# Kernel optimization log

Hardware: AMD Instinct MI355X
Metric: run time of the kernel (lower is better)

Reference implementation:

```python
import jax, jax.numpy as jnp
import numpy as np

# dims
N = 50000          # nodes
E = 400000         # edges
R = 32             # radial basis
F = 132            # features_dim
EV = 15            # sum(2l+1) for degrees [1,2,3]
H_INV, D_INV = 4, 33
H_EV, D_EV = 3, 44
REPEATS = np.array([3, 5, 7])            # 2l+1 per degree
ATT_NORM_INV = float(np.sqrt(D_INV))
ATT_NORM_EV = float(np.sqrt(D_EV))

# degree contraction matrix: (x*x) @ M sums squared m-components per degree -> [.., 3]
M_L0 = np.zeros((EV, 3), np.float32)
_off = 0
for _i, _r in enumerate(REPEATS):
    M_L0[_off:_off + _r, _i] = 1.0
    _off += _r
M_L0 = jnp.asarray(M_L0)


def _filter_net(rbf, ev_inv, rW1, rb1, rW2, rb2, eW1, eb1, eW2, eb2):
    # FilterNet with num_layers=2: silu(Linear) -> Linear(identity), same for ev path
    a = jax.nn.silu(rbf @ rW1 + rb1) @ rW2 + rb2
    e = jax.nn.silu(ev_inv @ eW1 + eb1) @ eW2 + eb2
    return a + e


def setup_inputs() -> dict:
    key = jax.random.key(0)
    ks = jax.random.split(key, 40)
    p = lambda i, shp, s=0.1: jax.random.normal(ks[i], shp, jnp.float32) * s
    inp = {
        'inv_features': jax.random.normal(ks[0], (N, F), jnp.float32),
        'ev_features': jax.random.normal(ks[1], (N, EV), jnp.float32),
        'rbf': jax.random.uniform(ks[2], (E, R), jnp.float32),
        'sh_vectors': jax.random.normal(ks[3], (E, EV), jnp.float32),
        'cutoffs': jax.random.uniform(ks[4], (E, 1), jnp.float32),
        'senders': jax.random.randint(ks[5], (E,), 0, N),
        'receivers': jax.random.randint(ks[6], (E,), 0, N),
        # attention weights
        'Wq_inv': p(7, (H_INV, D_INV, D_INV)),
        'Wk_inv': p(8, (H_INV, D_INV, D_INV)),
        'Wv_inv': p(9, (H_INV, D_INV, D_INV)),
        'Wq_ev': p(10, (H_EV, D_EV, D_EV)),
        'Wk_ev': p(11, (H_EV, D_EV, D_EV)),
        # filter net (inv branch)
        'fi_rW1': p(12, (R, F)), 'fi_rb1': p(13, (F,)),
        'fi_rW2': p(14, (F, F)), 'fi_rb2': p(15, (F,)),
        'fi_eW1': p(16, (3, F // 4)), 'fi_eb1': p(17, (F // 4,)),
        'fi_eW2': p(18, (F // 4, F)), 'fi_eb2': p(19, (F,)),
        # filter net (ev branch)
        'fe_rW1': p(20, (R, F)), 'fe_rb1': p(21, (F,)),
        'fe_rW2': p(22, (F, F)), 'fe_rb2': p(23, (F,)),
        'fe_eW1': p(24, (3, F // 4)), 'fe_eb1': p(25, (F // 4,)),
        'fe_eW2': p(26, (F // 4, F)), 'fe_eb2': p(27, (F,)),
        # interaction block linear: (F + len(degrees)) -> (F + len(degrees))
        'W_int': p(28, (F + 3, F + 3)), 'b_int': p(29, (F + 3,)),
    }
    return inp


def reference(inv_features, ev_features, rbf, sh_vectors, cutoffs,
              Wq_inv, Wk_inv, Wv_inv, Wq_ev, Wk_ev,
              fi_rW1, fi_rb1, fi_rW2, fi_rb2, fi_eW1, fi_eb1, fi_eW2, fi_eb2,
              fe_rW1, fe_rb1, fe_rW2, fe_rb2, fe_eW1, fe_eb1, fe_eW2, fe_eb2,
              W_int, b_int, senders, receivers):
    n = inv_features.shape[0]

    # --- Euclidean attention block ---
    ev_diff = ev_features[senders] - ev_features[receivers]          # [E, 15]
    ev_diff_inv = (ev_diff * ev_diff) @ M_L0                          # [E, 3] L0 contraction

    fw_inv = _filter_net(rbf, ev_diff_inv, fi_rW1, fi_rb1, fi_rW2, fi_rb2,
                         fi_eW1, fi_eb1, fi_eW2, fi_eb2).reshape(-1, H_INV, D_INV)
    fw_ev = _filter_net(rbf, ev_diff_inv, fe_rW1, fe_rb1, fe_rW2, fe_rb2,
                        fe_eW1, fe_eb1, fe_eW2, fe_eb2).reshape(-1, H_EV, D_EV)

    x_inv = inv_features.reshape(n, H_INV, D_INV)
    x_ev = inv_features.reshape(n, H_EV, D_EV)

    q_inv = jax.nn.silu(jnp.einsum('nhd,hde->nhe', x_inv, Wq_inv))[receivers]
    k_inv = jax.nn.silu(jnp.einsum('nhd,hde->nhe', x_inv, Wk_inv))[senders]
    v_inv = jnp.einsum('nhd,hde->nhe', x_inv, Wv_inv)[senders]
    q_ev = jax.nn.silu(jnp.einsum('nhd,hde->nhe', x_ev, Wq_ev))[receivers]
    k_ev = jax.nn.silu(jnp.einsum('nhd,hde->nhe', x_ev, Wk_ev))[senders]

    alpha_inv = (q_inv * k_inv * fw_inv).sum(-1) / ATT_NORM_INV       # [E, 4]
    alpha_ev = (q_ev * k_ev * fw_ev).sum(-1) / ATT_NORM_EV            # [E, 3]

    msg_inv = cutoffs[:, :, None] * alpha_inv[..., None] * v_inv      # [E, 4, 33]
    d_inv = jax.ops.segment_sum(msg_inv, receivers, num_segments=n).reshape(n, F)

    alpha_ev_full = jnp.repeat(alpha_ev, REPEATS, axis=-1, total_repeat_length=EV)
    msg_ev = cutoffs * alpha_ev_full * sh_vectors                      # [E, 15]
    d_ev = jax.ops.segment_sum(msg_ev, receivers, num_segments=n)

    inv1 = inv_features + d_inv
    ev1 = ev_features + d_ev

    # --- Interaction block ---
    ev1_inv = (ev1 * ev1) @ M_L0                                       # [N, 3]
    t = jnp.concatenate([inv1, ev1_inv], axis=-1) @ W_int + b_int      # [N, 135]
    d_inv2, b_ev = t[:, :F], t[:, F:]
    d_ev2 = jnp.repeat(b_ev, REPEATS, axis=-1, total_repeat_length=EV) * ev1

    return (inv1 + d_inv2, ev1 + d_ev2)
```

## Files before the change

### kernel.cpp

```cpp
#include <hip/hip_runtime.h>
#include <type_traits>

#define N_NODES 50000
#define N_EDGES 400000
#define R_DIM   32
#define F_DIM   132
#define EV_DIM  15
#define F_Q     33
#define INT_DIM 135
#define TE      32
#define NPB     32

#define RCP_NORM_INV 0.17407765595569785f
#define RCP_NORM_EV  0.15075567228888181f

typedef __attribute__((ext_vector_type(8))) short bf16x8;
typedef __attribute__((ext_vector_type(4))) float f32x4;

__device__ __forceinline__ float silu_f(float x) { return x / (1.f + __expf(-x)); }

__device__ __forceinline__ unsigned short f2bf(float x) {
    union { float f; unsigned u; } c; c.f = x;
    unsigned r = c.u + 0x7FFFu + ((c.u >> 16) & 1u);
    return (unsigned short)(r >> 16);
}

__device__ __forceinline__ float bf2f(unsigned short x) {
    union { unsigned u; float f; } c; c.u = (unsigned)x << 16;
    return c.f;
}

__global__ __launch_bounds__(256) void prep_w2_kernel(
    const float* __restrict__ fi_rW2, const float* __restrict__ fi_eW2,
    const float* __restrict__ fe_rW2, const float* __restrict__ fe_eW2,
    const float* __restrict__ fi_rb2, const float* __restrict__ fi_eb2,
    const float* __restrict__ fe_rb2, const float* __restrict__ fe_eb2,
    unsigned short* __restrict__ Bfrag, float* __restrict__ biasC)
{
    int t = blockIdx.x * 256 + threadIdx.x;
    if (t < 6912) {
        int l = t & 63, idx = t >> 6;
        int nt = idx % 9, kc = (idx / 9) % 6, f = idx / 54;
        const float* rW2 = f ? fe_rW2 : fi_rW2;
        const float* eW2 = f ? fe_eW2 : fi_eW2;
        int n = nt * 16 + (l & 15);
        unsigned short v[8];
        #pragma unroll
        for (int j = 0; j < 8; ++j) {
            int k = kc * 32 + (l >> 4) * 8 + j;
            float w = 0.f;
            if (n < F_DIM) {
                if (k < F_DIM) w = rW2[k * F_DIM + n];
                else if (k < F_DIM + F_Q) w = eW2[(k - F_DIM) * F_DIM + n];
            }
            v[j] = f2bf(w);
        }
        *(uint4*)&Bfrag[(size_t)t * 8] = *(const uint4*)v;
    }
    if (blockIdx.x == 0) {
        for (int i = threadIdx.x; i < 288; i += 256) {
            int f = i / 144, n = i % 144;
            const float* rb2 = f ? fe_rb2 : fi_rb2;
            const float* eb2 = f ? fe_eb2 : fi_eb2;
            biasC[i] = (n < F_DIM) ? (rb2[n] + eb2[n]) : 0.f;
        }
    }
}

__global__ __launch_bounds__(256) void prep_aux_kernel(
    const float* __restrict__ fi_rW1, const float* __restrict__ fe_rW1,
    const float* __restrict__ fi_rb1, const float* __restrict__ fi_eb1,
    const float* __restrict__ fe_rb1, const float* __restrict__ fe_eb1,
    const float* __restrict__ Wq_inv, const float* __restrict__ Wk_inv,
    const float* __restrict__ Wv_inv,
    const float* __restrict__ Wq_ev, const float* __restrict__ Wk_ev,
    unsigned short* __restrict__ B1frag, float* __restrict__ biasB1,
    unsigned short* __restrict__ Bnp)
{
    int t = blockIdx.x * 256 + threadIdx.x;
    if (t < 1536) {
        int l = t & 63, idx = t >> 6;
        int nt = idx % 12, f = idx / 12;
        const float* rW1 = f ? fe_rW1 : fi_rW1;
        int n = nt * 16 + (l & 15);
        unsigned short v[8];
        #pragma unroll
        for (int j = 0; j < 8; ++j) {
            int k = (l >> 4) * 8 + j;
            float w = (n < F_DIM) ? rW1[k * F_DIM + n] : 0.f;
            v[j] = f2bf(w);
        }
        *(uint4*)&B1frag[(size_t)t * 8] = *(const uint4*)v;
    } else if (t < 1920) {
        int i = t - 1536;
        int f = i / 192, n = i % 192;
        const float* rb1 = f ? fe_rb1 : fi_rb1;
        const float* eb1 = f ? fe_eb1 : fi_eb1;
        biasB1[i] = (n < F_DIM) ? rb1[n] : ((n < 165) ? eb1[n - F_DIM] : 0.f);
    } else if (t < 1920 + 6912) {
        int u = t - 1920;
        int l = u & 63, blk = u >> 6;
        int n = 0; const float* W = nullptr; int D = 0, h = 0, kc = 0;
        if (blk < 72) {
            int arr = blk / 24, wb = blk % 24;
            h = wb / 6; kc = (wb % 6) / 3; int nt = wb % 3;
            W = (arr == 0) ? Wq_inv : (arr == 1) ? Wk_inv : Wv_inv;
            D = 33; n = nt * 16 + (l & 15);
            W += h * 1089;
        } else {
            int b2 = blk - 72;
            int which = b2 / 18, wb = b2 % 18;
            h = wb / 6; kc = (wb % 6) / 3; int nt = wb % 3;
            W = which ? Wk_ev : Wq_ev;
            D = 44; n = nt * 16 + (l & 15);
            W += h * 1936;
        }
        unsigned short v[8];
        #pragma unroll
        for (int j = 0; j < 8; ++j) {
            int k = kc * 32 + (l >> 4) * 8 + j;
            float w = (k < D && n < D) ? W[k * D + n] : 0.f;
            v[j] = f2bf(w);
        }
        *(uint4*)&Bnp[(size_t)u * 8] = *(const uint4*)v;
    }
}

__global__ __launch_bounds__(256) void hist_kernel(
    const int* __restrict__ receivers, int* __restrict__ cnt)
{
    int i = blockIdx.x * 256 + threadIdx.x;
    if (i < N_EDGES) atomicAdd(&cnt[receivers[i]], 1);
}

__global__ __launch_bounds__(1024) void scan_tile_sum(
    const int* __restrict__ cnt, int* __restrict__ tsum)
{
    int idx = blockIdx.x * 1024 + threadIdx.x;
    int v = (idx < N_NODES) ? cnt[idx] : 0;
    for (int o = 32; o > 0; o >>= 1) v += __shfl_down(v, o);
    __shared__ int wsum[16];
    if ((threadIdx.x & 63) == 0) wsum[threadIdx.x >> 6] = v;
    __syncthreads();
    if (threadIdx.x == 0) {
        int s = 0;
        for (int i = 0; i < 16; ++i) s += wsum[i];
        tsum[blockIdx.x] = s;
    }
}

__global__ __launch_bounds__(64) void scan_base(
    const int* __restrict__ tsum, int* __restrict__ tbase)
{
    if (threadIdx.x == 0) {
        int run = 0;
        for (int i = 0; i < 49; ++i) { tbase[i] = run; run += tsum[i]; }
    }
}

__global__ __launch_bounds__(1024) void scan_tile(
    const int* __restrict__ cnt, const int* __restrict__ tbase,
    int* __restrict__ off, int* __restrict__ cursor)
{
    __shared__ int s[1024];
    int t = threadIdx.x;
    int idx = blockIdx.x * 1024 + t;
    int v = (idx < N_NODES) ? cnt[idx] : 0;
    s[t] = v;
    __syncthreads();
    for (int d = 1; d < 1024; d <<= 1) {
        int x = (t >= d) ? s[t - d] : 0;
        __syncthreads();
        s[t] += x;
        __syncthreads();
    }
    int o = tbase[blockIdx.x] + s[t] - v;
    if (idx < N_NODES) { off[idx] = o; cursor[idx] = o; }
    if (idx == 0) off[N_NODES] = N_EDGES;
}

__global__ __launch_bounds__(256) void scatter_kernel(
    const int* __restrict__ receivers, int* __restrict__ cursor,
    int* __restrict__ perm)
{
    int i = blockIdx.x * 256 + threadIdx.x;
    if (i < N_EDGES) {
        int pos = atomicAdd(&cursor[receivers[i]], 1);
        perm[pos] = i;
    }
}

__global__ __launch_bounds__(256) void node_proj_kernel(
    const float* __restrict__ x,
    const unsigned short* __restrict__ Bnp,
    unsigned short* __restrict__ q_inv, unsigned short* __restrict__ k_inv,
    float* __restrict__ v_inv,
    unsigned short* __restrict__ q_ev, unsigned short* __restrict__ k_ev)
{
    __shared__ __align__(16) unsigned short sx[NPB][456];
    const int node0 = blockIdx.x * NPB;
    const int tid = threadIdx.x;
    for (int i = tid; i < NPB * 448; i += 256) {
        int nd = i / 448, t = i % 448;
        int seg = t >> 6, d = t & 63;
        float v = 0.f;
        int gn = node0 + nd;
        if (gn < N_NODES) {
            if (seg < 4) { if (d < 33) v = x[(size_t)gn * F_DIM + seg * 33 + d]; }
            else         { int h = seg - 4; if (d < 44) v = x[(size_t)gn * F_DIM + h * 44 + d]; }
        }
        sx[nd][t] = f2bf(v);
    }
    __syncthreads();
    const int wv = tid >> 6, l = tid & 63, l15 = l & 15, g4 = l >> 4;
    const int half = wv & 1, m0 = (wv >> 1) * 16;
    const unsigned short* arow = &sx[m0 + l15][0];
    const unsigned short* Bl = Bnp + (size_t)l * 8;

    auto do_qk = [&](int arr, unsigned short* __restrict__ out) {
        const unsigned short* Ba = Bl + (size_t)arr * 24 * 512;
        #pragma unroll
        for (int h = 0; h < 4; ++h) {
            bf16x8 a0 = *(const bf16x8*)&arow[h * 64 + g4 * 8];
            bf16x8 a1 = *(const bf16x8*)&arow[h * 64 + 32 + g4 * 8];
            #pragma unroll
            for (int nt = 0; nt < 3; ++nt) {
                f32x4 c = {0.f, 0.f, 0.f, 0.f};
                c = __builtin_amdgcn_mfma_f32_16x16x32_bf16(
                        a0, *(const bf16x8*)(Ba + (size_t)((h * 2 + 0) * 3 + nt) * 512), c, 0, 0, 0);
                c = __builtin_amdgcn_mfma_f32_16x16x32_bf16(
                        a1, *(const bf16x8*)(Ba + (size_t)((h * 2 + 1) * 3 + nt) * 512), c, 0, 0, 0);
                int e = nt * 16 + l15;
                if (e < 33) {
                    #pragma unroll
                    for (int r = 0; r < 4; ++r) {
                        int gn = node0 + m0 + g4 * 4 + r;
                        if (gn < N_NODES)
                            out[(size_t)gn * F_DIM + h * 33 + e] = f2bf(silu_f(c[r]));
                    }
                }
            }
        }
    };
    auto do_v = [&](float* __restrict__ out) {
        const unsigned short* Ba = Bl + (size_t)2 * 24 * 512;
        #pragma unroll
        for (int h = 0; h < 4; ++h) {
            bf16x8 a0 = *(const bf16x8*)&arow[h * 64 + g4 * 8];
            bf16x8 a1 = *(const bf16x8*)&arow[h * 64 + 32 + g4 * 8];
            #pragma unroll
            for (int nt = 0; nt < 3; ++nt) {
                f32x4 c = {0.f, 0.f, 0.f, 0.f};
                c = __builtin_amdgcn_mfma_f32_16x16x32_bf16(
                        a0, *(const bf16x8*)(Ba + (size_t)((h * 2 + 0) * 3 + nt) * 512), c, 0, 0, 0);
                c = __builtin_amdgcn_mfma_f32_16x16x32_bf16(
                        a1, *(const bf16x8*)(Ba + (size_t)((h * 2 + 1) * 3 + nt) * 512), c, 0, 0, 0);
                int e = nt * 16 + l15;
                if (e < 33) {
                    #pragma unroll
                    for (int r = 0; r < 4; ++r) {
                        int gn = node0 + m0 + g4 * 4 + r;
                        if (gn < N_NODES)
                            out[(size_t)gn * F_DIM + h * 33 + e] = c[r];
                    }
                }
            }
        }
    };
    auto do_ev = [&](int which, unsigned short* __restrict__ out) {
        const unsigned short* Ba = Bl + (size_t)(72 + which * 18) * 512;
        #pragma unroll
        for (int h = 0; h < 3; ++h) {
            bf16x8 a0 = *(const bf16x8*)&arow[256 + h * 64 + g4 * 8];
            bf16x8 a1 = *(const bf16x8*)&arow[256 + h * 64 + 32 + g4 * 8];
            #pragma unroll
            for (int nt = 0; nt < 3; ++nt) {
                f32x4 c = {0.f, 0.f, 0.f, 0.f};
                c = __builtin_amdgcn_mfma_f32_16x16x32_bf16(
                        a0, *(const bf16x8*)(Ba + (size_t)((h * 2 + 0) * 3 + nt) * 512), c, 0, 0, 0);
                c = __builtin_amdgcn_mfma_f32_16x16x32_bf16(
                        a1, *(const bf16x8*)(Ba + (size_t)((h * 2 + 1) * 3 + nt) * 512), c, 0, 0, 0);
                int e = nt * 16 + l15;
                if (e < 44) {
                    #pragma unroll
                    for (int r = 0; r < 4; ++r) {
                        int gn = node0 + m0 + g4 * 4 + r;
                        if (gn < N_NODES)
                            out[(size_t)gn * F_DIM + h * 44 + e] = f2bf(silu_f(c[r]));
                    }
                }
            }
        }
    };
    if (half == 0) { do_qk(0, q_inv); do_qk(1, k_inv); }
    else           { do_v(v_inv); do_ev(0, q_ev); do_ev(1, k_ev); }
}

__global__ __launch_bounds__(256) void edge_alpha_kernel(
    const float* __restrict__ ev_feat, const float* __restrict__ rbf,
    const float* __restrict__ cutoffs,
    const int* __restrict__ senders, const int* __restrict__ receivers,
    const int* __restrict__ perm,
    const float* __restrict__ fi_eW1, const float* __restrict__ fe_eW1,
    const unsigned short* __restrict__ B1frag, const float* __restrict__ biasB1,
    const unsigned short* __restrict__ Bfrag, const float* __restrict__ biasC,
    const unsigned short* __restrict__ q_inv, const unsigned short* __restrict__ k_inv,
    const unsigned short* __restrict__ q_ev, const unsigned short* __restrict__ k_ev,
    float* __restrict__ galpha, int* __restrict__ gsnd)
{
    __shared__ __align__(16) unsigned short s_hid[2][TE][200];
    __shared__ __align__(16) unsigned short s_ain[TE][40];
    __shared__ float s_d2[TE][16];
    __shared__ float s_ei[3][TE];
    __shared__ float s_c[TE];
    __shared__ int s_snd[TE], s_rcv[TE], s_eid[TE];

    const int e0g = blockIdx.x * TE;
    const int tid = threadIdx.x;

    if (tid < TE) {
        int eid = perm[e0g + tid];
        s_eid[tid] = eid;
        int sn = senders[eid], rc = receivers[eid];
        s_snd[tid] = sn; s_rcv[tid] = rc;
        s_c[tid] = cutoffs[eid];
        gsnd[e0g + tid] = sn;
    }
    __syncthreads();
    for (int i = tid; i < TE * R_DIM; i += 256) {
        int e = i >> 5, k = i & 31;
        s_ain[e][k] = f2bf(rbf[(size_t)s_eid[e] * R_DIM + k]);
    }
    for (int i = tid; i < TE * EV_DIM; i += 256) {
        int e = i / EV_DIM, j = i - e * EV_DIM;
        float d = ev_feat[(size_t)s_snd[e] * EV_DIM + j]
                - ev_feat[(size_t)s_rcv[e] * EV_DIM + j];
        s_d2[e][j] = d * d;
    }
    __syncthreads();
    if (tid < TE * 3) {
        int e = tid / 3, k2 = tid - e * 3;
        int i0 = (k2 == 0) ? 0 : (k2 == 1) ? 3 : 8;
        int i1 = (k2 == 0) ? 3 : (k2 == 1) ? 8 : 15;
        float s = 0.f;
        for (int i = i0; i < i1; ++i) s += s_d2[e][i];
        s_ei[k2][e] = s;
    }
    __syncthreads();

    const int wv = tid >> 6, l = tid & 63;
    const int f = wv & 1, m0 = (wv >> 1) * 16;
    const int l15 = l & 15, g4 = l >> 4;

    int rcvr[4], sndr[4];
    #pragma unroll
    for (int r = 0; r < 4; ++r) {
        int e = m0 + g4 * 4 + r;
        rcvr[r] = s_rcv[e]; sndr[r] = s_snd[e];
    }

    {
        bf16x8 a1 = *(const bf16x8*)&s_ain[m0 + l15][g4 * 8];
        const unsigned short* B1f = B1frag + (size_t)f * 6144 + (size_t)l * 8;
        const float* eW1f = f ? fe_eW1 : fi_eW1;
        #pragma unroll
        for (int nt = 0; nt < 12; ++nt) {
            f32x4 c = {0.f, 0.f, 0.f, 0.f};
            bf16x8 b1 = *(const bf16x8*)(B1f + (size_t)nt * 512);
            c = __builtin_amdgcn_mfma_f32_16x16x32_bf16(a1, b1, c, 0, 0, 0);
            const int n = nt * 16 + l15;
            const float bias = biasB1[f * 192 + n];
            float w0 = 0.f, w1 = 0.f, w2 = 0.f;
            if (n >= F_DIM && n < 165) {
                w0 = eW1f[n - F_DIM];
                w1 = eW1f[F_Q + n - F_DIM];
                w2 = eW1f[2 * F_Q + n - F_DIM];
            }
            #pragma unroll
            for (int r = 0; r < 4; ++r) {
                int e = m0 + g4 * 4 + r;
                float eic = w0 * s_ei[0][e] + w1 * s_ei[1][e] + w2 * s_ei[2][e];
                float v = silu_f(c[r] + bias + eic);
                s_hid[f][e][n] = f2bf(v);
            }
        }
    }

    bf16x8 afr[6];
    {
        const unsigned short* hrow = &s_hid[f][m0 + l15][0];
        #pragma unroll
        for (int kc = 0; kc < 6; ++kc)
            afr[kc] = *(const bf16x8*)&hrow[kc * 32 + g4 * 8];
    }
    const unsigned short* Bf = Bfrag + (size_t)f * 54 * 512 + (size_t)l * 8;

    auto run = [&](auto FC) {
        constexpr int F_ = decltype(FC)::value;
        constexpr int NH = F_ ? 3 : 4;
        constexpr int DD = F_ ? 44 : 33;
        const unsigned short* qp = F_ ? q_ev : q_inv;
        const unsigned short* kp = F_ ? k_ev : k_inv;
        float part[NH][4];
        #pragma unroll
        for (int h = 0; h < NH; ++h)
            #pragma unroll
            for (int r = 0; r < 4; ++r) part[h][r] = 0.f;

        auto ldtile = [&](int nt, float (&bq)[4], float (&bk)[4]) {
            const int n = nt * 16 + l15;
            #pragma unroll
            for (int r = 0; r < 4; ++r) {
                float qv = 0.f, kv = 0.f;
                if (n < F_DIM) {
                    qv = bf2f(qp[(size_t)rcvr[r] * F_DIM + n]);
                    kv = bf2f(kp[(size_t)sndr[r] * F_DIM + n]);
                }
                bq[r] = qv; bk[r] = kv;
            }
        };

        float bq[2][4], bk[2][4];
        ldtile(0, bq[0], bk[0]);
        ldtile(1, bq[1], bk[1]);

        #pragma unroll
        for (int nt = 0; nt < 9; ++nt) {
            float cq[4], ck[4];
            #pragma unroll
            for (int r = 0; r < 4; ++r) { cq[r] = bq[nt & 1][r]; ck[r] = bk[nt & 1][r]; }
            if (nt + 2 < 9) ldtile(nt + 2, bq[nt & 1], bk[nt & 1]);

            f32x4 acc = {0.f, 0.f, 0.f, 0.f};
            #pragma unroll
            for (int kc = 0; kc < 6; ++kc) {
                bf16x8 bfr = *(const bf16x8*)(Bf + (size_t)(kc * 9 + nt) * 512);
                acc = __builtin_amdgcn_mfma_f32_16x16x32_bf16(afr[kc], bfr, acc, 0, 0, 0);
            }
            const int n = nt * 16 + l15;
            const bool nvalid = (n < F_DIM);
            const float bias = biasC[F_ * 144 + n];
            int h0v = (nt * 16) / DD;
            int bsp = (h0v + 1) * DD - nt * 16;
            #pragma unroll
            for (int r = 0; r < 4; ++r) {
                float p = 0.f;
                if (nvalid) p = (acc[r] + bias) * cq[r] * ck[r];
                if (bsp >= 16) {
                    part[h0v][r] += p;
                } else {
                    float plo = (l15 < bsp) ? p : 0.f;
                    part[h0v][r] += plo;
                    if (h0v + 1 < NH) part[h0v + 1][r] += (p - plo);
                }
            }
        }
        #pragma unroll
        for (int h = 0; h < NH; ++h) {
            #pragma unroll
            for (int r = 0; r < 4; ++r) {
                float v = part[h][r];
                v += __shfl_xor(v, 1);
                v += __shfl_xor(v, 2);
                v += __shfl_xor(v, 4);
                v += __shfl_xor(v, 8);
                if (l15 == 0) {
                    int e = m0 + g4 * 4 + r;
                    galpha[(size_t)(e0g + e) * 8 + (F_ ? 4 + h : h)] =
                        v * s_c[e] * (F_ ? RCP_NORM_EV : RCP_NORM_INV);
                }
            }
        }
    };
    if (f == 0) run(std::integral_constant<int, 0>{});
    else        run(std::integral_constant<int, 1>{});
}

__global__ __launch_bounds__(256) void gather_kernel(
    const float* __restrict__ v_inv, const float* __restrict__ sh_vec,
    const float* __restrict__ galpha,
    const int* __restrict__ gsnd, const int* __restrict__ perm,
    const int* __restrict__ off,
    float* __restrict__ a_inv, float* __restrict__ a_ev)
{
    int n = blockIdx.x * 4 + (threadIdx.x >> 6);
    int l = threadIdx.x & 63;
    int beg = off[n], end = off[n + 1];
    int c0 = l, c1 = l + 64, c2 = l + 128;
    int h0 = c0 / 33, h1 = c1 / 33;
    float acc0 = 0.f, acc1 = 0.f, acc2 = 0.f, aev = 0.f;
    int seg = (l < 3) ? 0 : (l < 8) ? 1 : 2;
    #pragma unroll 4
    for (int p = beg; p < end; ++p) {
        int snd = gsnd[p];
        const float* ga = &galpha[(size_t)p * 8];
        const float* vr = &v_inv[(size_t)snd * F_DIM];
        acc0 += ga[h0] * vr[c0];
        acc1 += ga[h1] * vr[c1];
        if (l < 4) acc2 += ga[3] * vr[c2];
        if (l < EV_DIM) {
            int eid = perm[p];
            aev += ga[4 + seg] * sh_vec[(size_t)eid * EV_DIM + l];
        }
    }
    float* dr = &a_inv[(size_t)n * F_DIM];
    dr[c0] = acc0; dr[c1] = acc1;
    if (l < 4) dr[c2] = acc2;
    if (l < EV_DIM) a_ev[(size_t)n * EV_DIM + l] = aev;
}

__global__ __launch_bounds__(256) void epilogue_kernel(
    const float* __restrict__ inv_feat, const float* __restrict__ ev_feat,
    const float* __restrict__ acc_inv, const float* __restrict__ acc_ev,
    const float* __restrict__ W_int, const float* __restrict__ b_int,
    float* __restrict__ out0, float* __restrict__ out1)
{
    const int NB = 16;
    __shared__ float s_in[NB][INT_DIM + 1];
    __shared__ float s_ev1[NB][EV_DIM + 1];
    __shared__ float s_b[NB][3];
    int n0 = blockIdx.x * NB;
    int tid = threadIdx.x;
    for (int i = tid; i < NB * F_DIM; i += 256) {
        int nb = i / F_DIM, j = i - nb * F_DIM;
        size_t idx = (size_t)(n0 + nb) * F_DIM + j;
        s_in[nb][j] = inv_feat[idx] + acc_inv[idx];
    }
    for (int i = tid; i < NB * EV_DIM; i += 256) {
        int nb = i / EV_DIM, j = i - nb * EV_DIM;
        size_t idx = (size_t)(n0 + nb) * EV_DIM + j;
        s_ev1[nb][j] = ev_feat[idx] + acc_ev[idx];
    }
    __syncthreads();
    if (tid < NB * 3) {
        int nb = tid / 3, k = tid - nb * 3;
        int i0 = (k == 0) ? 0 : (k == 1) ? 3 : 8;
        int i1 = (k == 0) ? 3 : (k == 1) ? 8 : 15;
        float s = 0.f;
        for (int i = i0; i < i1; ++i) { float v = s_ev1[nb][i]; s += v * v; }
        s_in[nb][F_DIM + k] = s;
    }
    __syncthreads();
    if (tid < INT_DIM) {
        int j = tid;
        float b = b_int[j];
        float acc[NB];
        #pragma unroll
        for (int nb = 0; nb < NB; ++nb) acc[nb] = b;
        for (int i = 0; i < INT_DIM; ++i) {
            float w = W_int[i * INT_DIM + j];
            #pragma unroll
            for (int nb = 0; nb < NB; ++nb) acc[nb] += s_in[nb][i] * w;
        }
        if (j < F_DIM) {
            #pragma unroll
            for (int nb = 0; nb < NB; ++nb)
                out0[(size_t)(n0 + nb) * F_DIM + j] = s_in[nb][j] + acc[nb];
        } else {
            #pragma unroll
            for (int nb = 0; nb < NB; ++nb)
                s_b[nb][j - F_DIM] = acc[nb];
        }
    }
    __syncthreads();
    for (int i = tid; i < NB * EV_DIM; i += 256) {
        int nb = i / EV_DIM, ii = i - nb * EV_DIM;
        int seg = (ii < 3) ? 0 : (ii < 8) ? 1 : 2;
        out1[(size_t)(n0 + nb) * EV_DIM + ii] = s_ev1[nb][ii] * (1.f + s_b[nb][seg]);
    }
}

extern "C" void kernel_launch(void* const* d_in, const int* in_sizes, int n_in,
                              void* d_out, int out_size, void* d_ws, size_t ws_size,
                              hipStream_t stream)
{
    const float* inv_feat  = (const float*)d_in[0];
    const float* ev_feat   = (const float*)d_in[1];
    const float* rbf       = (const float*)d_in[2];
    const float* sh_vec    = (const float*)d_in[3];
    const float* cutoffs   = (const float*)d_in[4];
    const int*   senders   = (const int*)d_in[5];
    const int*   receivers = (const int*)d_in[6];
    const float* Wq_inv = (const float*)d_in[7];
    const float* Wk_inv = (const float*)d_in[8];
    const float* Wv_inv = (const float*)d_in[9];
    const float* Wq_ev  = (const float*)d_in[10];
    const float* Wk_ev  = (const float*)d_in[11];
    const float* fi_rW1 = (const float*)d_in[12];
    const float* fi_rb1 = (const float*)d_in[13];
    const float* fi_rW2 = (const float*)d_in[14];
    const float* fi_rb2 = (const float*)d_in[15];
    const float* fi_eW1 = (const float*)d_in[16];
    const float* fi_eb1 = (const float*)d_in[17];
    const float* fi_eW2 = (const float*)d_in[18];
    const float* fi_eb2 = (const float*)d_in[19];
    const float* fe_rW1 = (const float*)d_in[20];
    const float* fe_rb1 = (const float*)d_in[21];
    const float* fe_rW2 = (const float*)d_in[22];
    const float* fe_rb2 = (const float*)d_in[23];
    const float* fe_eW1 = (const float*)d_in[24];
    const float* fe_eb1 = (const float*)d_in[25];
    const float* fe_eW2 = (const float*)d_in[26];
    const float* fe_eb2 = (const float*)d_in[27];
    const float* W_int  = (const float*)d_in[28];
    const float* b_int  = (const float*)d_in[29];

    const size_t NF = (size_t)N_NODES * F_DIM;
    float* ws    = (float*)d_ws;
    float* v_inv = ws;
    float* a_inv = ws + NF;
    float* a_ev  = ws + 2 * NF;
    float* galpha = a_ev + (size_t)N_NODES * EV_DIM;
    int*   perm   = (int*)(galpha + (size_t)N_EDGES * 8);
    int*   gsnd   = perm + N_EDGES;
    int*   cnt    = gsnd + N_EDGES;
    int*   off    = cnt + N_NODES;
    int*   cursor = off + (N_NODES + 4);
    unsigned short* Bfrag  = (unsigned short*)(cursor + N_NODES);
    float*          biasC  = (float*)(Bfrag + 55296);
    unsigned short* B1frag = (unsigned short*)(biasC + 288);
    float*          biasB1 = (float*)(B1frag + 12288);
    unsigned short* Bnp    = (unsigned short*)(biasB1 + 384);
    int* tsum  = (int*)(Bnp + 55296);
    int* tbase = tsum + 64;
    unsigned short* q_inv = (unsigned short*)(tbase + 64);
    unsigned short* k_inv = q_inv + NF;
    unsigned short* q_ev  = k_inv + NF;
    unsigned short* k_ev  = q_ev + NF;

    float* out0 = (float*)d_out;
    float* out1 = out0 + NF;

    hipMemsetAsync(cnt, 0, N_NODES * sizeof(int), stream);
    hist_kernel<<<(N_EDGES + 255) / 256, 256, 0, stream>>>(receivers, cnt);
    scan_tile_sum<<<49, 1024, 0, stream>>>(cnt, tsum);
    scan_base<<<1, 64, 0, stream>>>(tsum, tbase);
    scan_tile<<<49, 1024, 0, stream>>>(cnt, tbase, off, cursor);
    scatter_kernel<<<(N_EDGES + 255) / 256, 256, 0, stream>>>(receivers, cursor, perm);

    prep_w2_kernel<<<27, 256, 0, stream>>>(
        fi_rW2, fi_eW2, fe_rW2, fe_eW2,
        fi_rb2, fi_eb2, fe_rb2, fe_eb2, Bfrag, biasC);

    prep_aux_kernel<<<35, 256, 0, stream>>>(
        fi_rW1, fe_rW1, fi_rb1, fi_eb1, fe_rb1, fe_eb1,
        Wq_inv, Wk_inv, Wv_inv, Wq_ev, Wk_ev,
        B1frag, biasB1, Bnp);

    node_proj_kernel<<<(N_NODES + NPB - 1) / NPB, 256, 0, stream>>>(
        inv_feat, Bnp, q_inv, k_inv, v_inv, q_ev, k_ev);

    edge_alpha_kernel<<<N_EDGES / TE, 256, 0, stream>>>(
        ev_feat, rbf, cutoffs, senders, receivers, perm,
        fi_eW1, fe_eW1, B1frag, biasB1, Bfrag, biasC,
        q_inv, k_inv, q_ev, k_ev,
        galpha, gsnd);

    gather_kernel<<<N_NODES / 4, 256, 0, stream>>>(
        v_inv, sh_vec, galpha, gsnd, perm, off, a_inv, a_ev);

    epilogue_kernel<<<N_NODES / 16, 256, 0, stream>>>(
        inv_feat, ev_feat, a_inv, a_ev, W_int, b_int, out0, out1);
}
```

Measured before the change: 812.5 us.

## Stage q*k products in shared memory via vectorized cooperative gathers

The per-lane scalar bf16 gathers of q[receiver] and k[sender] inside the MFMA tile loop are replaced. A block-wide cooperative pass now loads both with 8-byte vector loads, multiplies them, and stores the bf16 q*k product into the reused s_hid shared buffer. The epilogue then reads a single LDS value per element. This is meant to cut scattered narrow global loads and register pressure, at the cost of two extra barriers and an extra bf16 rounding of the q*k product.

```diff
diff --git a/kernel.cpp b/kernel.cpp
--- a/kernel.cpp
+++ b/kernel.cpp
@@ -10,6 +10,7 @@
 #define INT_DIM 135
 #define TE      32
 #define NPB     32
+#define QK_STRIDE 140
 
 #define RCP_NORM_INV 0.17407765595569785f
 #define RCP_NORM_EV  0.15075567228888181f
@@ -352,13 +353,6 @@
     const int f = wv & 1, m0 = (wv >> 1) * 16;
     const int l15 = l & 15, g4 = l >> 4;
 
-    int rcvr[4], sndr[4];
-    #pragma unroll
-    for (int r = 0; r < 4; ++r) {
-        int e = m0 + g4 * 4 + r;
-        rcvr[r] = s_rcv[e]; sndr[r] = s_snd[e];
-    }
-
     {
         bf16x8 a1 = *(const bf16x8*)&s_ain[m0 + l15][g4 * 8];
         const unsigned short* B1f = B1frag + (size_t)f * 6144 + (size_t)l * 8;
@@ -393,44 +387,44 @@
         for (int kc = 0; kc < 6; ++kc)
             afr[kc] = *(const bf16x8*)&hrow[kc * 32 + g4 * 8];
     }
+    __syncthreads();
+
+    unsigned short* s_qk = &s_hid[0][0][0];
+    {
+        for (int i = tid; i < 2 * TE * 33; i += 256) {
+            int c = i % 33, e = (i / 33) % TE, b = i / (33 * TE);
+            const unsigned short* qp = b ? q_ev : q_inv;
+            const unsigned short* kp = b ? k_ev : k_inv;
+            int qrow = s_rcv[e], krow = s_snd[e];
+            uint2 qv = *(const uint2*)(qp + (size_t)qrow * F_DIM + c * 4);
+            uint2 kv = *(const uint2*)(kp + (size_t)krow * F_DIM + c * 4);
+            float p0 = bf2f((unsigned short)(qv.x & 0xffff)) * bf2f((unsigned short)(kv.x & 0xffff));
+            float p1 = bf2f((unsigned short)(qv.x >> 16))    * bf2f((unsigned short)(kv.x >> 16));
+            float p2 = bf2f((unsigned short)(qv.y & 0xffff)) * bf2f((unsigned short)(kv.y & 0xffff));
+            float p3 = bf2f((unsigned short)(qv.y >> 16))    * bf2f((unsigned short)(kv.y >> 16));
+            uint2 pv;
+            pv.x = (unsigned)f2bf(p0) | ((unsigned)f2bf(p1) << 16);
+            pv.y = (unsigned)f2bf(p2) | ((unsigned)f2bf(p3) << 16);
+            *(uint2*)(s_qk + (size_t)(b * TE + e) * QK_STRIDE + c * 4) = pv;
+        }
+    }
+    __syncthreads();
+
     const unsigned short* Bf = Bfrag + (size_t)f * 54 * 512 + (size_t)l * 8;
+    const unsigned short* qkbase = s_qk + (size_t)f * TE * QK_STRIDE;
 
     auto run = [&](auto FC) {
         constexpr int F_ = decltype(FC)::value;
         constexpr int NH = F_ ? 3 : 4;
         constexpr int DD = F_ ? 44 : 33;
-        const unsigned short* qp = F_ ? q_ev : q_inv;
-        const unsigned short* kp = F_ ? k_ev : k_inv;
         float part[NH][4];
         #pragma unroll
         for (int h = 0; h < NH; ++h)
             #pragma unroll
             for (int r = 0; r < 4; ++r) part[h][r] = 0.f;
 
-        auto ldtile = [&](int nt, float (&bq)[4], float (&bk)[4]) {
-            const int n = nt * 16 + l15;
-            #pragma unroll
-            for (int r = 0; r < 4; ++r) {
-                float qv = 0.f, kv = 0.f;
-                if (n < F_DIM) {
-                    qv = bf2f(qp[(size_t)rcvr[r] * F_DIM + n]);
-                    kv = bf2f(kp[(size_t)sndr[r] * F_DIM + n]);
-                }
-                bq[r] = qv; bk[r] = kv;
-            }
-        };
-
-        float bq[2][4], bk[2][4];
-        ldtile(0, bq[0], bk[0]);
-        ldtile(1, bq[1], bk[1]);
-
         #pragma unroll
         for (int nt = 0; nt < 9; ++nt) {
-            float cq[4], ck[4];
-            #pragma unroll
-            for (int r = 0; r < 4; ++r) { cq[r] = bq[nt & 1][r]; ck[r] = bk[nt & 1][r]; }
-            if (nt + 2 < 9) ldtile(nt + 2, bq[nt & 1], bk[nt & 1]);
-
             f32x4 acc = {0.f, 0.f, 0.f, 0.f};
             #pragma unroll
             for (int kc = 0; kc < 6; ++kc) {
@@ -444,8 +438,12 @@
             int bsp = (h0v + 1) * DD - nt * 16;
             #pragma unroll
             for (int r = 0; r < 4; ++r) {
+                int e = m0 + g4 * 4 + r;
                 float p = 0.f;
-                if (nvalid) p = (acc[r] + bias) * cq[r] * ck[r];
+                if (nvalid) {
+                    float qk = bf2f(qkbase[(size_t)e * QK_STRIDE + n]);
+                    p = (acc[r] + bias) * qk;
+                }
                 if (bsp >= 16) {
                     part[h0v][r] += p;
                 } else {
```

Result: slower. 841.1 us (+3.5%).

## Fuse message aggregation into edge-alpha kernel with segmented reduction and atomics

Applied to the files above, without the earlier changes.

Removes the separate gather kernel and its galpha/gsnd round-trip. Attention weights now stay in shared memory, and the edge kernel accumulates v*alpha and sh*alpha per receiver run over its receiver-sorted tile. It stores directly when a receiver's whole segment lies inside the tile and uses atomicAdd otherwise, which needs an added memset of the accumulators. v_inv is also stored as bf16 to halve gather traffic, and silu uses a hardware reciprocal. The trade-offs are lower precision for v, atomic contention, and extra serial per-thread work over 32 edges in the edge kernel.

```diff
diff --git a/kernel.cpp b/kernel.cpp
--- a/kernel.cpp
+++ b/kernel.cpp
@@ -17,7 +17,9 @@
 typedef __attribute__((ext_vector_type(8))) short bf16x8;
 typedef __attribute__((ext_vector_type(4))) float f32x4;
 
-__device__ __forceinline__ float silu_f(float x) { return x / (1.f + __expf(-x)); }
+__device__ __forceinline__ float silu_f(float x) {
+    return x * __builtin_amdgcn_rcpf(1.f + __expf(-x));
+}
 
 __device__ __forceinline__ unsigned short f2bf(float x) {
     union { float f; unsigned u; } c; c.f = x;
@@ -194,7 +196,7 @@
     const float* __restrict__ x,
     const unsigned short* __restrict__ Bnp,
     unsigned short* __restrict__ q_inv, unsigned short* __restrict__ k_inv,
-    float* __restrict__ v_inv,
+    unsigned short* __restrict__ v_bf,
     unsigned short* __restrict__ q_ev, unsigned short* __restrict__ k_ev)
 {
     __shared__ __align__(16) unsigned short sx[NPB][456];
@@ -217,7 +219,7 @@
     const unsigned short* arow = &sx[m0 + l15][0];
     const unsigned short* Bl = Bnp + (size_t)l * 8;
 
-    auto do_qk = [&](int arr, unsigned short* __restrict__ out) {
+    auto do_inv = [&](int arr, unsigned short* __restrict__ out, bool dosilu) {
         const unsigned short* Ba = Bl + (size_t)arr * 24 * 512;
         #pragma unroll
         for (int h = 0; h < 4; ++h) {
@@ -235,33 +237,11 @@
                     #pragma unroll
                     for (int r = 0; r < 4; ++r) {
                         int gn = node0 + m0 + g4 * 4 + r;
-                        if (gn < N_NODES)
-                            out[(size_t)gn * F_DIM + h * 33 + e] = f2bf(silu_f(c[r]));
-                    }
-                }
-            }
-        }
-    };
-    auto do_v = [&](float* __restrict__ out) {
-        const unsigned short* Ba = Bl + (size_t)2 * 24 * 512;
-        #pragma unroll
-        for (int h = 0; h < 4; ++h) {
-            bf16x8 a0 = *(const bf16x8*)&arow[h * 64 + g4 * 8];
-            bf16x8 a1 = *(const bf16x8*)&arow[h * 64 + 32 + g4 * 8];
-            #pragma unroll
-            for (int nt = 0; nt < 3; ++nt) {
-                f32x4 c = {0.f, 0.f, 0.f, 0.f};
-                c = __builtin_amdgcn_mfma_f32_16x16x32_bf16(
-                        a0, *(const bf16x8*)(Ba + (size_t)((h * 2 + 0) * 3 + nt) * 512), c, 0, 0, 0);
-                c = __builtin_amdgcn_mfma_f32_16x16x32_bf16(
-                        a1, *(const bf16x8*)(Ba + (size_t)((h * 2 + 1) * 3 + nt) * 512), c, 0, 0, 0);
-                int e = nt * 16 + l15;
-                if (e < 33) {
-                    #pragma unroll
-                    for (int r = 0; r < 4; ++r) {
-                        int gn = node0 + m0 + g4 * 4 + r;
-                        if (gn < N_NODES)
-                            out[(size_t)gn * F_DIM + h * 33 + e] = c[r];
+                        if (gn < N_NODES) {
+                            float v = c[r];
+                            if (dosilu) v = silu_f(v);
+                            out[(size_t)gn * F_DIM + h * 33 + e] = f2bf(v);
+                        }
                     }
                 }
             }
@@ -292,28 +272,31 @@
             }
         }
     };
-    if (half == 0) { do_qk(0, q_inv); do_qk(1, k_inv); }
-    else           { do_v(v_inv); do_ev(0, q_ev); do_ev(1, k_ev); }
+    if (half == 0) { do_inv(0, q_inv, true); do_inv(1, k_inv, true); }
+    else           { do_inv(2, v_bf, false); do_ev(0, q_ev); do_ev(1, k_ev); }
 }
 
 __global__ __launch_bounds__(256) void edge_alpha_kernel(
     const float* __restrict__ ev_feat, const float* __restrict__ rbf,
-    const float* __restrict__ cutoffs,
+    const float* __restrict__ cutoffs, const float* __restrict__ sh_vec,
     const int* __restrict__ senders, const int* __restrict__ receivers,
-    const int* __restrict__ perm,
+    const int* __restrict__ perm, const int* __restrict__ off,
     const float* __restrict__ fi_eW1, const float* __restrict__ fe_eW1,
     const unsigned short* __restrict__ B1frag, const float* __restrict__ biasB1,
     const unsigned short* __restrict__ Bfrag, const float* __restrict__ biasC,
     const unsigned short* __restrict__ q_inv, const unsigned short* __restrict__ k_inv,
     const unsigned short* __restrict__ q_ev, const unsigned short* __restrict__ k_ev,
-    float* __restrict__ galpha, int* __restrict__ gsnd)
+    const unsigned short* __restrict__ v_bf,
+    float* __restrict__ a_inv, float* __restrict__ a_ev)
 {
     __shared__ __align__(16) unsigned short s_hid[2][TE][200];
     __shared__ __align__(16) unsigned short s_ain[TE][40];
     __shared__ float s_d2[TE][16];
     __shared__ float s_ei[3][TE];
     __shared__ float s_c[TE];
+    __shared__ float s_alpha[TE][8];
     __shared__ int s_snd[TE], s_rcv[TE], s_eid[TE];
+    __shared__ unsigned char s_glast[TE], s_gcomp[TE];
 
     const int e0g = blockIdx.x * TE;
     const int tid = threadIdx.x;
@@ -324,7 +307,6 @@
         int sn = senders[eid], rc = receivers[eid];
         s_snd[tid] = sn; s_rcv[tid] = rc;
         s_c[tid] = cutoffs[eid];
-        gsnd[e0g + tid] = sn;
     }
     __syncthreads();
     for (int i = tid; i < TE * R_DIM; i += 256) {
@@ -345,6 +327,11 @@
         float s = 0.f;
         for (int i = i0; i < i1; ++i) s += s_d2[e][i];
         s_ei[k2][e] = s;
+    } else if (tid < TE * 3 + TE) {
+        int e = tid - TE * 3;
+        int rcv = s_rcv[e];
+        s_glast[e] = (e == TE - 1) || (s_rcv[e + 1] != rcv);
+        s_gcomp[e] = (off[rcv] >= e0g) && (off[rcv + 1] <= e0g + TE);
     }
     __syncthreads();
 
@@ -466,7 +453,7 @@
                 v += __shfl_xor(v, 8);
                 if (l15 == 0) {
                     int e = m0 + g4 * 4 + r;
-                    galpha[(size_t)(e0g + e) * 8 + (F_ ? 4 + h : h)] =
+                    s_alpha[e][F_ ? 4 + h : h] =
                         v * s_c[e] * (F_ ? RCP_NORM_EV : RCP_NORM_INV);
                 }
             }
@@ -474,39 +461,40 @@
     };
     if (f == 0) run(std::integral_constant<int, 0>{});
     else        run(std::integral_constant<int, 1>{});
-}
-
-__global__ __launch_bounds__(256) void gather_kernel(
-    const float* __restrict__ v_inv, const float* __restrict__ sh_vec,
-    const float* __restrict__ galpha,
-    const int* __restrict__ gsnd, const int* __restrict__ perm,
-    const int* __restrict__ off,
-    float* __restrict__ a_inv, float* __restrict__ a_ev)
-{
-    int n = blockIdx.x * 4 + (threadIdx.x >> 6);
-    int l = threadIdx.x & 63;
-    int beg = off[n], end = off[n + 1];
-    int c0 = l, c1 = l + 64, c2 = l + 128;
-    int h0 = c0 / 33, h1 = c1 / 33;
-    float acc0 = 0.f, acc1 = 0.f, acc2 = 0.f, aev = 0.f;
-    int seg = (l < 3) ? 0 : (l < 8) ? 1 : 2;
-    #pragma unroll 4
-    for (int p = beg; p < end; ++p) {
-        int snd = gsnd[p];
-        const float* ga = &galpha[(size_t)p * 8];
-        const float* vr = &v_inv[(size_t)snd * F_DIM];
-        acc0 += ga[h0] * vr[c0];
-        acc1 += ga[h1] * vr[c1];
-        if (l < 4) acc2 += ga[3] * vr[c2];
-        if (l < EV_DIM) {
-            int eid = perm[p];
-            aev += ga[4 + seg] * sh_vec[(size_t)eid * EV_DIM + l];
-        }
-    }
-    float* dr = &a_inv[(size_t)n * F_DIM];
-    dr[c0] = acc0; dr[c1] = acc1;
-    if (l < 4) dr[c2] = acc2;
-    if (l < EV_DIM) a_ev[(size_t)n * EV_DIM + l] = aev;
+
+    __syncthreads();
+
+    if (tid < F_DIM) {
+        const int c = tid;
+        const int h = c / 33;
+        float acc = 0.f;
+        #pragma unroll 4
+        for (int e = 0; e < TE; ++e) {
+            float vv = bf2f(v_bf[(size_t)s_snd[e] * F_DIM + c]);
+            acc += s_alpha[e][h] * vv;
+            if (s_glast[e]) {
+                float* dst = &a_inv[(size_t)s_rcv[e] * F_DIM + c];
+                if (s_gcomp[e]) *dst = acc;
+                else atomicAdd(dst, acc);
+                acc = 0.f;
+            }
+        }
+    } else if (tid < F_DIM + EV_DIM) {
+        const int j = tid - F_DIM;
+        const int seg = (j < 3) ? 0 : (j < 8) ? 1 : 2;
+        float acc = 0.f;
+        #pragma unroll 4
+        for (int e = 0; e < TE; ++e) {
+            float sv = sh_vec[(size_t)s_eid[e] * EV_DIM + j];
+            acc += s_alpha[e][4 + seg] * sv;
+            if (s_glast[e]) {
+                float* dst = &a_ev[(size_t)s_rcv[e] * EV_DIM + j];
+                if (s_gcomp[e]) *dst = acc;
+                else atomicAdd(dst, acc);
+                acc = 0.f;
+            }
+        }
+    }
 }
 
 __global__ __launch_bounds__(256) void epilogue_kernel(
@@ -606,14 +594,12 @@
     const float* b_int  = (const float*)d_in[29];
 
     const size_t NF = (size_t)N_NODES * F_DIM;
+    const size_t NE = (size_t)N_NODES * EV_DIM;
     float* ws    = (float*)d_ws;
-    float* v_inv = ws;
-    float* a_inv = ws + NF;
-    float* a_ev  = ws + 2 * NF;
-    float* galpha = a_ev + (size_t)N_NODES * EV_DIM;
-    int*   perm   = (int*)(galpha + (size_t)N_EDGES * 8);
-    int*   gsnd   = perm + N_EDGES;
-    int*   cnt    = gsnd + N_EDGES;
+    float* a_inv = ws;
+    float* a_ev  = ws + NF;
+    int*   perm   = (int*)(a_ev + NE);
+    int*   cnt    = perm + N_EDGES;
     int*   off    = cnt + N_NODES;
     int*   cursor = off + (N_NODES + 4);
     unsigned short* Bfrag  = (unsigned short*)(cursor + N_NODES);
@@ -627,11 +613,13 @@
     unsigned short* k_inv = q_inv + NF;
     unsigned short* q_ev  = k_inv + NF;
     unsigned short* k_ev  = q_ev + NF;
+    unsigned short* v_bf  = k_ev + NF;
 
     float* out0 = (float*)d_out;
     float* out1 = out0 + NF;
 
     hipMemsetAsync(cnt, 0, N_NODES * sizeof(int), stream);
+    hipMemsetAsync(a_inv, 0, (NF + NE) * sizeof(float), stream);
     hist_kernel<<<(N_EDGES + 255) / 256, 256, 0, stream>>>(receivers, cnt);
     scan_tile_sum<<<49, 1024, 0, stream>>>(cnt, tsum);
     scan_base<<<1, 64, 0, stream>>>(tsum, tbase);
@@ -648,16 +636,13 @@
         B1frag, biasB1, Bnp);
 
     node_proj_kernel<<<(N_NODES + NPB - 1) / NPB, 256, 0, stream>>>(
-        inv_feat, Bnp, q_inv, k_inv, v_inv, q_ev, k_ev);
+        inv_feat, Bnp, q_inv, k_inv, v_bf, q_ev, k_ev);
 
     edge_alpha_kernel<<<N_EDGES / TE, 256, 0, stream>>>(
-        ev_feat, rbf, cutoffs, senders, receivers, perm,
+        ev_feat, rbf, cutoffs, sh_vec, senders, receivers, perm, off,
         fi_eW1, fe_eW1, B1frag, biasB1, Bfrag, biasC,
-        q_inv, k_inv, q_ev, k_ev,
-        galpha, gsnd);
-
-    gather_kernel<<<N_NODES / 4, 256, 0, stream>>>(
-        v_inv, sh_vec, galpha, gsnd, perm, off, a_inv, a_ev);
+        q_inv, k_inv, q_ev, k_ev, v_bf,
+        a_inv, a_ev);
 
     epilogue_kernel<<<N_NODES / 16, 256, 0, stream>>>(
         inv_feat, ev_feat, a_inv, a_ev, W_int, b_int, out0, out1);
```

New measurement: 1.002 ms. 1.23x slower.

## Store v projections in bf16 and run interaction matmul on MFMA

Applied to the files above, without the earlier changes.

Three changes. The node projection now writes v_inv as bf16 instead of fp32, which halves the bytes the gather kernel reads per sender row. The epilogue's scalar fp32 135x135 matmul is replaced by bf16 MFMA tiles, fed by a W_int fragment layout that the prep kernel builds. silu also switches to a hardware reciprocal. Together these lower precision for v and for the interaction layer, which risks accuracy drift.

```diff
diff --git a/kernel.cpp b/kernel.cpp
--- a/kernel.cpp
+++ b/kernel.cpp
@@ -17,7 +17,9 @@
 typedef __attribute__((ext_vector_type(8))) short bf16x8;
 typedef __attribute__((ext_vector_type(4))) float f32x4;
 
-__device__ __forceinline__ float silu_f(float x) { return x / (1.f + __expf(-x)); }
+__device__ __forceinline__ float silu_f(float x) {
+    return x * __builtin_amdgcn_rcpf(1.f + __expf(-x));
+}
 
 __device__ __forceinline__ unsigned short f2bf(float x) {
     union { float f; unsigned u; } c; c.f = x;
@@ -35,7 +37,9 @@
     const float* __restrict__ fe_rW2, const float* __restrict__ fe_eW2,
     const float* __restrict__ fi_rb2, const float* __restrict__ fi_eb2,
     const float* __restrict__ fe_rb2, const float* __restrict__ fe_eb2,
-    unsigned short* __restrict__ Bfrag, float* __restrict__ biasC)
+    const float* __restrict__ W_int,
+    unsigned short* __restrict__ Bfrag, float* __restrict__ biasC,
+    unsigned short* __restrict__ Wfrag_int)
 {
     int t = blockIdx.x * 256 + threadIdx.x;
     if (t < 6912) {
@@ -56,6 +60,19 @@
             v[j] = f2bf(w);
         }
         *(uint4*)&Bfrag[(size_t)t * 8] = *(const uint4*)v;
+    } else if (t < 6912 + 2880) {
+        int u = t - 6912;
+        int l = u & 63, idx = u >> 6;
+        int nt = idx % 9, kc = idx / 9;
+        int n = nt * 16 + (l & 15);
+        unsigned short v[8];
+        #pragma unroll
+        for (int j = 0; j < 8; ++j) {
+            int k = kc * 32 + (l >> 4) * 8 + j;
+            float w = (k < INT_DIM && n < INT_DIM) ? W_int[k * INT_DIM + n] : 0.f;
+            v[j] = f2bf(w);
+        }
+        *(uint4*)&Wfrag_int[(size_t)u * 8] = *(const uint4*)v;
     }
     if (blockIdx.x == 0) {
         for (int i = threadIdx.x; i < 288; i += 256) {
@@ -194,7 +211,7 @@
     const float* __restrict__ x,
     const unsigned short* __restrict__ Bnp,
     unsigned short* __restrict__ q_inv, unsigned short* __restrict__ k_inv,
-    float* __restrict__ v_inv,
+    unsigned short* __restrict__ v_bf,
     unsigned short* __restrict__ q_ev, unsigned short* __restrict__ k_ev)
 {
     __shared__ __align__(16) unsigned short sx[NPB][456];
@@ -217,7 +234,7 @@
     const unsigned short* arow = &sx[m0 + l15][0];
     const unsigned short* Bl = Bnp + (size_t)l * 8;
 
-    auto do_qk = [&](int arr, unsigned short* __restrict__ out) {
+    auto do_inv = [&](int arr, unsigned short* __restrict__ out, bool dosilu) {
         const unsigned short* Ba = Bl + (size_t)arr * 24 * 512;
         #pragma unroll
         for (int h = 0; h < 4; ++h) {
@@ -235,33 +252,11 @@
                     #pragma unroll
                     for (int r = 0; r < 4; ++r) {
                         int gn = node0 + m0 + g4 * 4 + r;
-                        if (gn < N_NODES)
-                            out[(size_t)gn * F_DIM + h * 33 + e] = f2bf(silu_f(c[r]));
-                    }
-                }
-            }
-        }
-    };
-    auto do_v = [&](float* __restrict__ out) {
-        const unsigned short* Ba = Bl + (size_t)2 * 24 * 512;
-        #pragma unroll
-        for (int h = 0; h < 4; ++h) {
-            bf16x8 a0 = *(const bf16x8*)&arow[h * 64 + g4 * 8];
-            bf16x8 a1 = *(const bf16x8*)&arow[h * 64 + 32 + g4 * 8];
-            #pragma unroll
-            for (int nt = 0; nt < 3; ++nt) {
-                f32x4 c = {0.f, 0.f, 0.f, 0.f};
-                c = __builtin_amdgcn_mfma_f32_16x16x32_bf16(
-                        a0, *(const bf16x8*)(Ba + (size_t)((h * 2 + 0) * 3 + nt) * 512), c, 0, 0, 0);
-                c = __builtin_amdgcn_mfma_f32_16x16x32_bf16(
-                        a1, *(const bf16x8*)(Ba + (size_t)((h * 2 + 1) * 3 + nt) * 512), c, 0, 0, 0);
-                int e = nt * 16 + l15;
-                if (e < 33) {
-                    #pragma unroll
-                    for (int r = 0; r < 4; ++r) {
-                        int gn = node0 + m0 + g4 * 4 + r;
-                        if (gn < N_NODES)
-                            out[(size_t)gn * F_DIM + h * 33 + e] = c[r];
+                        if (gn < N_NODES) {
+                            float v = c[r];
+                            if (dosilu) v = silu_f(v);
+                            out[(size_t)gn * F_DIM + h * 33 + e] = f2bf(v);
+                        }
                     }
                 }
             }
@@ -292,8 +287,8 @@
             }
         }
     };
-    if (half == 0) { do_qk(0, q_inv); do_qk(1, k_inv); }
-    else           { do_v(v_inv); do_ev(0, q_ev); do_ev(1, k_ev); }
+    if (half == 0) { do_inv(0, q_inv, true); do_inv(1, k_inv, true); }
+    else           { do_inv(2, v_bf, false); do_ev(0, q_ev); do_ev(1, k_ev); }
 }
 
 __global__ __launch_bounds__(256) void edge_alpha_kernel(
@@ -477,7 +472,7 @@
 }
 
 __global__ __launch_bounds__(256) void gather_kernel(
-    const float* __restrict__ v_inv, const float* __restrict__ sh_vec,
+    const unsigned short* __restrict__ v_bf, const float* __restrict__ sh_vec,
     const float* __restrict__ galpha,
     const int* __restrict__ gsnd, const int* __restrict__ perm,
     const int* __restrict__ off,
@@ -494,10 +489,10 @@
     for (int p = beg; p < end; ++p) {
         int snd = gsnd[p];
         const float* ga = &galpha[(size_t)p * 8];
-        const float* vr = &v_inv[(size_t)snd * F_DIM];
-        acc0 += ga[h0] * vr[c0];
-        acc1 += ga[h1] * vr[c1];
-        if (l < 4) acc2 += ga[3] * vr[c2];
+        const unsigned short* vr = &v_bf[(size_t)snd * F_DIM];
+        acc0 += ga[h0] * bf2f(vr[c0]);
+        acc1 += ga[h1] * bf2f(vr[c1]);
+        if (l < 4) acc2 += ga[3] * bf2f(vr[c2]);
         if (l < EV_DIM) {
             int eid = perm[p];
             aev += ga[4 + seg] * sh_vec[(size_t)eid * EV_DIM + l];
@@ -512,11 +507,12 @@
 __global__ __launch_bounds__(256) void epilogue_kernel(
     const float* __restrict__ inv_feat, const float* __restrict__ ev_feat,
     const float* __restrict__ acc_inv, const float* __restrict__ acc_ev,
-    const float* __restrict__ W_int, const float* __restrict__ b_int,
+    const unsigned short* __restrict__ Wfrag_int, const float* __restrict__ b_int,
     float* __restrict__ out0, float* __restrict__ out1)
 {
     const int NB = 16;
     __shared__ float s_in[NB][INT_DIM + 1];
+    __shared__ __align__(16) unsigned short s_inb[NB][168];
     __shared__ float s_ev1[NB][EV_DIM + 1];
     __shared__ float s_b[NB][3];
     int n0 = blockIdx.x * NB;
@@ -541,25 +537,30 @@
         s_in[nb][F_DIM + k] = s;
     }
     __syncthreads();
-    if (tid < INT_DIM) {
-        int j = tid;
-        float b = b_int[j];
-        float acc[NB];
-        #pragma unroll
-        for (int nb = 0; nb < NB; ++nb) acc[nb] = b;
-        for (int i = 0; i < INT_DIM; ++i) {
-            float w = W_int[i * INT_DIM + j];
-            #pragma unroll
-            for (int nb = 0; nb < NB; ++nb) acc[nb] += s_in[nb][i] * w;
-        }
-        if (j < F_DIM) {
-            #pragma unroll
-            for (int nb = 0; nb < NB; ++nb)
-                out0[(size_t)(n0 + nb) * F_DIM + j] = s_in[nb][j] + acc[nb];
-        } else {
-            #pragma unroll
-            for (int nb = 0; nb < NB; ++nb)
-                s_b[nb][j - F_DIM] = acc[nb];
+    for (int i = tid; i < NB * 160; i += 256) {
+        int nb = i / 160, j = i - nb * 160;
+        s_inb[nb][j] = f2bf((j < INT_DIM) ? s_in[nb][j] : 0.f);
+    }
+    __syncthreads();
+    const int wv = tid >> 6, l = tid & 63, l15 = l & 15, g4 = l >> 4;
+    for (int nt = wv; nt < 9; nt += 4) {
+        f32x4 c = {0.f, 0.f, 0.f, 0.f};
+        #pragma unroll
+        for (int kc = 0; kc < 5; ++kc) {
+            bf16x8 a = *(const bf16x8*)&s_inb[l15][kc * 32 + g4 * 8];
+            bf16x8 b = *(const bf16x8*)(Wfrag_int + (size_t)((kc * 9 + nt) * 64 + l) * 8);
+            c = __builtin_amdgcn_mfma_f32_16x16x32_bf16(a, b, c, 0, 0, 0);
+        }
+        int j = nt * 16 + l15;
+        float bias = (j < INT_DIM) ? b_int[j] : 0.f;
+        #pragma unroll
+        for (int r = 0; r < 4; ++r) {
+            int nb = g4 * 4 + r;
+            float val = c[r] + bias;
+            if (j < F_DIM)
+                out0[(size_t)(n0 + nb) * F_DIM + j] = s_in[nb][j] + val;
+            else if (j < INT_DIM)
+                s_b[nb][j - F_DIM] = val;
         }
     }
     __syncthreads();
@@ -606,11 +607,11 @@
     const float* b_int  = (const float*)d_in[29];
 
     const size_t NF = (size_t)N_NODES * F_DIM;
+    const size_t NE = (size_t)N_NODES * EV_DIM;
     float* ws    = (float*)d_ws;
-    float* v_inv = ws;
-    float* a_inv = ws + NF;
-    float* a_ev  = ws + 2 * NF;
-    float* galpha = a_ev + (size_t)N_NODES * EV_DIM;
+    float* a_inv = ws;
+    float* a_ev  = ws + NF;
+    float* galpha = a_ev + NE;
     int*   perm   = (int*)(galpha + (size_t)N_EDGES * 8);
     int*   gsnd   = perm + N_EDGES;
     int*   cnt    = gsnd + N_EDGES;
@@ -627,6 +628,8 @@
     unsigned short* k_inv = q_inv + NF;
     unsigned short* q_ev  = k_inv + NF;
     unsigned short* k_ev  = q_ev + NF;
+    unsigned short* v_bf  = k_ev + NF;
+    unsigned short* Wfrag_int = v_bf + NF;
 
     float* out0 = (float*)d_out;
     float* out1 = out0 + NF;
@@ -638,9 +641,9 @@
     scan_tile<<<49, 1024, 0, stream>>>(cnt, tbase, off, cursor);
     scatter_kernel<<<(N_EDGES + 255) / 256, 256, 0, stream>>>(receivers, cursor, perm);
 
-    prep_w2_kernel<<<27, 256, 0, stream>>>(
+    prep_w2_kernel<<<39, 256, 0, stream>>>(
         fi_rW2, fi_eW2, fe_rW2, fe_eW2,
-        fi_rb2, fi_eb2, fe_rb2, fe_eb2, Bfrag, biasC);
+        fi_rb2, fi_eb2, fe_rb2, fe_eb2, W_int, Bfrag, biasC, Wfrag_int);
 
     prep_aux_kernel<<<35, 256, 0, stream>>>(
         fi_rW1, fe_rW1, fi_rb1, fi_eb1, fe_rb1, fe_eb1,
@@ -648,7 +651,7 @@
         B1frag, biasB1, Bnp);
 
     node_proj_kernel<<<(N_NODES + NPB - 1) / NPB, 256, 0, stream>>>(
-        inv_feat, Bnp, q_inv, k_inv, v_inv, q_ev, k_ev);
+        inv_feat, Bnp, q_inv, k_inv, v_bf, q_ev, k_ev);
 
     edge_alpha_kernel<<<N_EDGES / TE, 256, 0, stream>>>(
         ev_feat, rbf, cutoffs, senders, receivers, perm,
@@ -657,8 +660,8 @@
         galpha, gsnd);
 
     gather_kernel<<<N_NODES / 4, 256, 0, stream>>>(
-        v_inv, sh_vec, galpha, gsnd, perm, off, a_inv, a_ev);
+        v_bf, sh_vec, galpha, gsnd, perm, off, a_inv, a_ev);
 
     epilogue_kernel<<<N_NODES / 16, 256, 0, stream>>>(
-        inv_feat, ev_feat, a_inv, a_ev, W_int, b_int, out0, out1);
-}
+        inv_feat, ev_feat, a_inv, a_ev, Wfrag_int, b_int, out0, out1);
+}
```

Result: faster. 720.0 us (-11.4%).
